# Performance work log

Measured on AMD Instinct MI355X. Metric: run time of the kernel, lower is better.

Reference implementation:

```python
import jax, jax.numpy as jnp
import numpy as np

N = 10000       # nodes
E = 160000      # edges
D_IN = 256      # in_channels (node feature dim)
H1, C = 8, 32   # conv1: 8 heads x 32 -> 256; conv2: 1 head x 32
MSG = 128       # msg_dim
TD = 128        # time encoder out_channels
ED = MSG + TD   # edge_dim = 256
HC1 = H1 * C    # 256


def _lin(key, shape, scale=0.05):
    return jax.random.normal(key, shape, dtype=jnp.float32) * scale


def setup_inputs() -> dict:
    key = jax.random.key(0)
    ks = jax.random.split(key, 32)
    inp = {}
    inp["x"] = jax.random.normal(ks[0], (N, D_IN), dtype=jnp.float32)
    inp["last_update"] = jax.random.uniform(ks[1], (N,), jnp.float32, 0.0, 1000.0)
    inp["edge_index"] = jax.random.randint(ks[2], (2, E), 0, N)
    inp["t"] = jax.random.uniform(ks[3], (E,), jnp.float32, 0.0, 1000.0)
    inp["msg"] = jax.random.normal(ks[4], (E, MSG), dtype=jnp.float32)
    # TimeEncoder: Linear(1, TD) then cos
    inp["time_w"] = _lin(ks[5], (TD, 1), 0.1)
    inp["time_b"] = jnp.zeros((TD,), jnp.float32)
    # conv1 (TransformerConv in=256, heads=8, per-head 32, edge_dim=256, concat=True)
    inp["Wq1"] = _lin(ks[6], (D_IN, HC1)); inp["bq1"] = jnp.zeros((HC1,), jnp.float32)
    inp["Wk1"] = _lin(ks[7], (D_IN, HC1)); inp["bk1"] = jnp.zeros((HC1,), jnp.float32)
    inp["Wv1"] = _lin(ks[8], (D_IN, HC1)); inp["bv1"] = jnp.zeros((HC1,), jnp.float32)
    inp["We1"] = _lin(ks[9], (ED, HC1))   # lin_edge has no bias in PyG
    inp["Ws1"] = _lin(ks[10], (D_IN, HC1)); inp["bs1"] = jnp.zeros((HC1,), jnp.float32)
    # conv2 (in=256, heads=1, per-head 32, concat=False)
    inp["Wq2"] = _lin(ks[11], (HC1, C)); inp["bq2"] = jnp.zeros((C,), jnp.float32)
    inp["Wk2"] = _lin(ks[12], (HC1, C)); inp["bk2"] = jnp.zeros((C,), jnp.float32)
    inp["Wv2"] = _lin(ks[13], (HC1, C)); inp["bv2"] = jnp.zeros((C,), jnp.float32)
    inp["We2"] = _lin(ks[14], (ED, C))
    inp["Ws2"] = _lin(ks[15], (HC1, C)); inp["bs2"] = jnp.zeros((C,), jnp.float32)
    return inp


def transformer_conv(x, src, dst, edge_attr, Wq, bq, Wk, bk, Wv, bv, We, Ws, bs, heads, ch, concat):
    n = x.shape[0]
    q = (x @ Wq + bq).reshape(n, heads, ch)
    k = (x @ Wk + bk).reshape(n, heads, ch)
    v = (x @ Wv + bv).reshape(n, heads, ch)
    e = (edge_attr @ We).reshape(-1, heads, ch)       # [E,H,C]
    ke = k[src] + e                                    # key_j + edge
    ve = v[src] + e                                    # value_j + edge
    alpha = jnp.einsum('ehc,ehc->eh', q[dst], ke) / jnp.sqrt(jnp.float32(ch))
    # segment softmax over incoming edges of each destination node
    amax = jax.ops.segment_max(alpha, dst, num_segments=n)   # -inf for empty segs
    ex = jnp.exp(alpha - amax[dst])
    den = jax.ops.segment_sum(ex, dst, num_segments=n)
    attn = ex / (den[dst] + 1e-16)                     # [E,H]
    out = jax.ops.segment_sum(attn[:, :, None] * ve, dst, num_segments=n)  # [N,H,C]
    out = out.reshape(n, heads * ch) if concat else out.mean(axis=1)
    return out + (x @ Ws + bs)                         # root skip connection


def reference(x, last_update, edge_index, t, msg, time_w, time_b,
              Wq1, bq1, Wk1, bk1, Wv1, bv1, We1, Ws1, bs1,
              Wq2, bq2, Wk2, bk2, Wv2, bv2, We2, Ws2, bs2):
    src, dst = edge_index[0], edge_index[1]
    rel_t = last_update[src] - t                       # [E]
    rel_t_enc = jnp.cos(rel_t[:, None] * time_w[:, 0][None, :] + time_b)  # [E,TD]
    edge_attr = jnp.concatenate([rel_t_enc, msg], axis=-1)                # [E,ED]
    h = jax.nn.relu(transformer_conv(x, src, dst, edge_attr,
                                     Wq1, bq1, Wk1, bk1, Wv1, bv1, We1, Ws1, bs1,
                                     H1, C, True))
    out = jax.nn.relu(transformer_conv(h, src, dst, edge_attr,
                                       Wq2, bq2, Wk2, bk2, Wv2, bv2, We2, Ws2, bs2,
                                       1, C, False))
    return out
```

## Files before the change

kernel.cpp:

```cpp
#include <hip/hip_runtime.h>
#include <math.h>

#define N_NODES 10000
#define N_EDGES 160000
#define RT1 157
#define RTE 2500
#define CONVX_T (RT1 * 64 * 32)
#define MAXSEG 16
#define SEGSTRIDE 576

static inline int ceildiv(int a, int b) { return (a + b - 1) / b; }

typedef float f32x4 __attribute__((ext_vector_type(4)));
typedef short bf16x8 __attribute__((ext_vector_type(8)));

__device__ __forceinline__ unsigned short f2bf(float f) {
  unsigned int u = __builtin_bit_cast(unsigned int, f);
  u += 0x7FFFu + ((u >> 16) & 1u);
  return (unsigned short)(u >> 16);
}
__device__ __forceinline__ float bf2f(unsigned short h) {
  unsigned int u = ((unsigned int)h) << 16;
  return __builtin_bit_cast(float, u);
}

__global__ void count_kernel(const int* __restrict__ dstp, int* __restrict__ deg, int E) {
  for (int i = blockIdx.x * blockDim.x + threadIdx.x; i < E; i += gridDim.x * blockDim.x)
    atomicAdd(&deg[dstp[i]], 1);
}

__global__ void scan_kernel(const int* __restrict__ deg, int* __restrict__ rowptr, int n) {
  __shared__ int part[1024];
  const int tid = threadIdx.x;
  const int CHK = 10;
  int base = tid * CHK;
  int loc[CHK];
  int s = 0;
#pragma unroll
  for (int j = 0; j < CHK; ++j) {
    int idx = base + j;
    int v = (idx < n) ? deg[idx] : 0;
    loc[j] = s; s += v;
  }
  part[tid] = s;
  __syncthreads();
  for (int off = 1; off < 1024; off <<= 1) {
    int y = (tid >= off) ? part[tid - off] : 0;
    __syncthreads();
    part[tid] += y;
    __syncthreads();
  }
  int pre = tid ? part[tid - 1] : 0;
#pragma unroll
  for (int j = 0; j < CHK; ++j) {
    int idx = base + j;
    if (idx < n) rowptr[idx] = pre + loc[j];
  }
  if (tid == 1023) rowptr[n] = part[1023];
}

__global__ void scatter_kernel(const float* __restrict__ lu, const float* __restrict__ tt,
                               const int* __restrict__ srcp, const int* __restrict__ dstp,
                               const int* __restrict__ rowptr, int* __restrict__ fill,
                               int* __restrict__ srcs, int* __restrict__ dsts,
                               int* __restrict__ eidA, float* __restrict__ rel_s, int E) {
  for (int e = blockIdx.x * blockDim.x + threadIdx.x; e < E; e += gridDim.x * blockDim.x) {
    int d = dstp[e], s = srcp[e];
    int pos = atomicAdd(&fill[d], 1);
    int slot = rowptr[d] + pos;
    srcs[slot] = s;
    dsts[slot] = d;
    eidA[slot] = e;
    rel_s[slot] = lu[s] - tt[e];
  }
}

__device__ __forceinline__ void wstore(const float* __restrict__ W, unsigned short* __restrict__ out,
                                       int Nin, int n_off, int NFtot, int k, int c) {
  int gc = n_off + c;
  int ks=k>>5, kg=(k>>3)&3, j=k&7, nf=gc>>4, ic=gc&15;
  out[(size_t)(ks*NFtot+nf)*512 + (ic+16*kg)*8 + j] = f2bf(W[(size_t)k*Nin + c]);
}

__global__ void conv_all_kernel(const float* __restrict__ x, unsigned short* __restrict__ xa,
                                const float* Wq1, const float* Wk1, const float* Wv1, const float* Ws1,
                                const float* We1, const float* Wq2, const float* Wk2, const float* Wv2,
                                const float* Ws2, const float* We2,
                                const float* bq1, const float* bk1, const float* bv1, const float* bs1,
                                const float* bq2, const float* bk2, const float* bv2, const float* bs2,
                                unsigned short* W1f, unsigned short* We1f, unsigned short* W2f,
                                unsigned short* We2f, float* bcat1, float* bcat2) {
  int t0 = blockIdx.x * blockDim.x + threadIdx.x;
  if (t0 < CONVX_T) {
    int i = t0 >> 5, k8 = t0 & 31;
    union { uint4 q; unsigned short s[8]; } u;
    if (i < N_NODES) {
      const float4* px = (const float4*)(x + (size_t)i * 256 + k8 * 8);
      float4 f0 = px[0], f1 = px[1];
      u.s[0]=f2bf(f0.x); u.s[1]=f2bf(f0.y); u.s[2]=f2bf(f0.z); u.s[3]=f2bf(f0.w);
      u.s[4]=f2bf(f1.x); u.s[5]=f2bf(f1.y); u.s[6]=f2bf(f1.z); u.s[7]=f2bf(f1.w);
    } else {
      u.q = make_uint4(0,0,0,0);
    }
    int rt=i>>6, rf=(i>>4)&3, ir=i&15, ks=k8>>2, kg=k8&3;
    *(uint4*)&xa[(size_t)rt*16384 + ks*2048 + rf*512 + (ir+16*kg)*8] = u.q;
    return;
  }
  int t = t0 - CONVX_T;
  if (t < 262144) {
    int w = t >> 16, r = t & 65535, k = r >> 8, c = r & 255;
    const float* W = (w == 0) ? Wq1 : (w == 1) ? Wk1 : (w == 2) ? Wv1 : Ws1;
    wstore(W, W1f, 256, w * 256, 64, k, c);
  } else if (t < 327680) {
    int r = t - 262144, k = r >> 8, c = r & 255;
    wstore(We1, We1f, 256, 0, 16, k, c);
  } else if (t < 360448) {
    int r = t - 327680, w = r >> 13, r2 = r & 8191, k = r2 >> 5, c = r2 & 31;
    const float* W = (w == 0) ? Wq2 : (w == 1) ? Wk2 : (w == 2) ? Wv2 : Ws2;
    wstore(W, W2f, 32, w * 32, 8, k, c);
  } else if (t < 368640) {
    int r = t - 360448, k = r >> 5, c = r & 31;
    wstore(We2, We2f, 32, 0, 4, k, c);
  } else if (t < 369792) {
    int r = t - 368640;
    if (r < 1024) {
      const float* b = (r < 256) ? bq1 : (r < 512) ? bk1 : (r < 768) ? bv1 : bs1;
      bcat1[r] = b[r & 255];
    } else {
      int r2 = r - 1024;
      const float* b = (r2 < 32) ? bq2 : (r2 < 64) ? bk2 : (r2 < 96) ? bv2 : bs2;
      bcat2[r2] = b[r2 & 31];
    }
  }
}

__global__ __launch_bounds__(512, 4)
void node1_gemm(const unsigned short* __restrict__ xa, const unsigned short* __restrict__ W1f,
                const float* __restrict__ bcat1, float* __restrict__ qf,
                unsigned short* __restrict__ kvb, float* __restrict__ sf) {
  __shared__ char ldsraw[32768];
  uint4* lds4 = (uint4*)ldsraw;
  const int tid = threadIdx.x;
  const int wid = tid >> 6, lane = tid & 63;
  const int fr0 = (lane >> 4) * 4;
  const int fc0 = lane & 15;
  const int rt0 = blockIdx.x % RT1;
  const int y = blockIdx.x / RT1;
  const int phase = rt0 & 7;

#pragma unroll
  for (int s = 0; s < 4; ++s)
    lds4[tid + s * 512] = *(const uint4*)(xa + (size_t)rt0 * 16384 + (size_t)(tid + s * 512) * 8);
  __syncthreads();

  f32x4 acc[4][2];
#pragma unroll
  for (int i = 0; i < 4; ++i)
#pragma unroll
    for (int j = 0; j < 2; ++j) acc[i][j] = (f32x4){0.f, 0.f, 0.f, 0.f};

  bf16x8 aN0, aN1, aN2, aN3, bN0, bN1;
  {
    const int ks = phase;
    aN0 = *(const bf16x8*)&lds4[ks * 256 + 0 * 64 + lane];
    aN1 = *(const bf16x8*)&lds4[ks * 256 + 1 * 64 + lane];
    aN2 = *(const bf16x8*)&lds4[ks * 256 + 2 * 64 + lane];
    aN3 = *(const bf16x8*)&lds4[ks * 256 + 3 * 64 + lane];
    bN0 = *(const bf16x8*)(W1f + ((size_t)(ks * 64 + y * 16 + wid * 2 + 0)) * 512 + (size_t)lane * 8);
    bN1 = *(const bf16x8*)(W1f + ((size_t)(ks * 64 + y * 16 + wid * 2 + 1)) * 512 + (size_t)lane * 8);
  }
#pragma unroll
  for (int ksi = 0; ksi < 8; ++ksi) {
    bf16x8 aC0 = aN0, aC1 = aN1, aC2 = aN2, aC3 = aN3;
    bf16x8 bC0 = bN0, bC1 = bN1;
    if (ksi < 7) {
      const int ks2 = (ksi + 1) ^ phase;
      aN0 = *(const bf16x8*)&lds4[ks2 * 256 + 0 * 64 + lane];
      aN1 = *(const bf16x8*)&lds4[ks2 * 256 + 1 * 64 + lane];
      aN2 = *(const bf16x8*)&lds4[ks2 * 256 + 2 * 64 + lane];
      aN3 = *(const bf16x8*)&lds4[ks2 * 256 + 3 * 64 + lane];
      bN0 = *(const bf16x8*)(W1f + ((size_t)(ks2 * 64 + y * 16 + wid * 2 + 0)) * 512 + (size_t)lane * 8);
      bN1 = *(const bf16x8*)(W1f + ((size_t)(ks2 * 64 + y * 16 + wid * 2 + 1)) * 512 + (size_t)lane * 8);
    }
    acc[0][0] = __builtin_amdgcn_mfma_f32_16x16x32_bf16(aC0, bC0, acc[0][0], 0, 0, 0);
    acc[1][0] = __builtin_amdgcn_mfma_f32_16x16x32_bf16(aC1, bC0, acc[1][0], 0, 0, 0);
    acc[2][0] = __builtin_amdgcn_mfma_f32_16x16x32_bf16(aC2, bC0, acc[2][0], 0, 0, 0);
    acc[3][0] = __builtin_amdgcn_mfma_f32_16x16x32_bf16(aC3, bC0, acc[3][0], 0, 0, 0);
    acc[0][1] = __builtin_amdgcn_mfma_f32_16x16x32_bf16(aC0, bC1, acc[0][1], 0, 0, 0);
    acc[1][1] = __builtin_amdgcn_mfma_f32_16x16x32_bf16(aC1, bC1, acc[1][1], 0, 0, 0);
    acc[2][1] = __builtin_amdgcn_mfma_f32_16x16x32_bf16(aC2, bC1, acc[2][1], 0, 0, 0);
    acc[3][1] = __builtin_amdgcn_mfma_f32_16x16x32_bf16(aC3, bC1, acc[3][1], 0, 0, 0);
  }

  bool bf16path;
  void* dstp_; int cstr_, dc0_, bcol0_;
  if (y == 0)      { bf16path = false; dstp_ = qf;  cstr_ = 256; dc0_ = 0;   bcol0_ = 0; }
  else if (y == 1) { bf16path = true;  dstp_ = kvb; cstr_ = 512; dc0_ = 0;   bcol0_ = 256; }
  else if (y == 2) { bf16path = true;  dstp_ = kvb; cstr_ = 512; dc0_ = 256; bcol0_ = 512; }
  else             { bf16path = false; dstp_ = sf;  cstr_ = 256; dc0_ = 0;   bcol0_ = 768; }
  if (!bf16path) {
    float* dst = (float*)dstp_;
    const int row0 = rt0 * 64 + fr0;
#pragma unroll
    for (int cf = 0; cf < 2; ++cf) {
      int c = wid * 32 + cf * 16 + fc0;
      float bv = bcat1[bcol0_ + c];
#pragma unroll
      for (int rf = 0; rf < 4; ++rf) {
#pragma unroll
        for (int j = 0; j < 4; ++j) {
          int r = row0 + rf * 16 + j;
          if (r < N_NODES) dst[(size_t)r * cstr_ + c] = acc[rf][cf][j] + bv;
        }
      }
    }
  } else {
    __syncthreads();
    unsigned short* cl = (unsigned short*)ldsraw;
    unsigned short* dst = (unsigned short*)dstp_;
    for (int pass = 0; pass < 4; ++pass) {
      if ((wid >> 1) == pass) {
#pragma unroll
        for (int cf = 0; cf < 2; ++cf) {
          int c = (wid & 1) * 32 + cf * 16 + fc0;
          float bv = bcat1[bcol0_ + pass * 64 + c];
#pragma unroll
          for (int rf = 0; rf < 4; ++rf)
#pragma unroll
            for (int j = 0; j < 4; ++j)
              cl[(fr0 + rf * 16 + j) * 72 + c] = f2bf(acc[rf][cf][j] + bv);
        }
      }
      __syncthreads();
      {
        int row = tid >> 3, cc = (tid & 7) * 8;
        int gr = rt0 * 64 + row;
        if (gr < N_NODES)
          *(uint4*)&dst[(size_t)gr * cstr_ + dc0_ + pass * 64 + cc] = *(const uint4*)&cl[row * 72 + cc];
      }
      __syncthreads();
    }
  }
}

__global__ __launch_bounds__(512, 4)
void edge_fused(const float* __restrict__ qf, const unsigned short* __restrict__ kvb,
                const unsigned short* __restrict__ We1f, const unsigned short* __restrict__ We2f,
                char* __restrict__ segrec, unsigned short* __restrict__ e2b,
                const float* __restrict__ rel_s, const float* __restrict__ tw,
                const float* __restrict__ tb, const float* __restrict__ msg,
                const int* __restrict__ eidA, const int* __restrict__ srcsA,
                const int* __restrict__ dstsA, const int* __restrict__ rowptr) {
  __shared__ char ldsraw[38912];
  uint4* lds4 = (uint4*)ldsraw;
  unsigned short* e1t = (unsigned short*)ldsraw;
  int* dseg     = (int*)(ldsraw + 33280);
  int* sseg     = (int*)(ldsraw + 33536);
  unsigned short* cl2 = (unsigned short*)(ldsraw + 33792);

  const int tid = threadIdx.x;
  const int wid = tid >> 6, lane = tid & 63;
  const int bx = blockIdx.x;
  const int fr0 = (lane >> 4) * 4;
  const int fc0 = lane & 15;
  const int rt0 = bx;
  const int phase = bx & 7;

  {
    const int rem = tid & 255;
    const int ksh = tid >> 8;
    const int arf = rem >> 6, ar2 = rem & 63, air = ar2 & 15, akg = ar2 >> 4;
    const int slot = rt0 * 64 + arf * 16 + air;
    float rl = rel_s[slot];
    int eorg = eidA[slot];
    if (tid < 64) {
      dseg[tid] = dstsA[rt0 * 64 + tid];
      sseg[tid] = srcsA[rt0 * 64 + tid];
    }
#pragma unroll
    for (int s = 0; s < 2; ++s) {
      int ks = ksh + s * 2;
      int k8 = ks * 4 + akg;
      const float4* twp = (const float4*)(tw + k8 * 8);
      const float4* tbp = (const float4*)(tb + k8 * 8);
      float4 w0 = twp[0], w1 = twp[1], b0 = tbp[0], b1 = tbp[1];
      union { uint4 q; unsigned short us[8]; } u;
      u.us[0]=f2bf(__cosf(rl*w0.x+b0.x)); u.us[1]=f2bf(__cosf(rl*w0.y+b0.y));
      u.us[2]=f2bf(__cosf(rl*w0.z+b0.z)); u.us[3]=f2bf(__cosf(rl*w0.w+b0.w));
      u.us[4]=f2bf(__cosf(rl*w1.x+b1.x)); u.us[5]=f2bf(__cosf(rl*w1.y+b1.y));
      u.us[6]=f2bf(__cosf(rl*w1.z+b1.z)); u.us[7]=f2bf(__cosf(rl*w1.w+b1.w));
      lds4[ks * 256 + rem] = u.q;
    }
#pragma unroll
    for (int s = 0; s < 2; ++s) {
      int ks = 4 + ksh + s * 2;
      int k8 = ks * 4 + akg;
      const float4* pm = (const float4*)(msg + (size_t)eorg * 128 + (size_t)(k8 - 16) * 8);
      float4 f0 = pm[0], f1 = pm[1];
      union { uint4 q; unsigned short us[8]; } u;
      u.us[0]=f2bf(f0.x); u.us[1]=f2bf(f0.y); u.us[2]=f2bf(f0.z); u.us[3]=f2bf(f0.w);
      u.us[4]=f2bf(f1.x); u.us[5]=f2bf(f1.y); u.us[6]=f2bf(f1.z); u.us[7]=f2bf(f1.w);
      lds4[ks * 256 + rem] = u.q;
    }
  }
  __syncthreads();

  f32x4 acc[4][2];
  f32x4 acc2[4];
#pragma unroll
  for (int i = 0; i < 4; ++i) {
    acc2[i] = (f32x4){0.f, 0.f, 0.f, 0.f};
#pragma unroll
    for (int j = 0; j < 2; ++j) acc[i][j] = (f32x4){0.f, 0.f, 0.f, 0.f};
  }

  bf16x8 aN0, aN1, aN2, aN3, bN0, bN1, b2N;
  {
    const int ks = phase;
    aN0 = *(const bf16x8*)&lds4[ks * 256 + 0 * 64 + lane];
    aN1 = *(const bf16x8*)&lds4[ks * 256 + 1 * 64 + lane];
    aN2 = *(const bf16x8*)&lds4[ks * 256 + 2 * 64 + lane];
    aN3 = *(const bf16x8*)&lds4[ks * 256 + 3 * 64 + lane];
    bN0 = *(const bf16x8*)(We1f + ((size_t)(ks * 16 + wid * 2 + 0)) * 512 + (size_t)lane * 8);
    bN1 = *(const bf16x8*)(We1f + ((size_t)(ks * 16 + wid * 2 + 1)) * 512 + (size_t)lane * 8);
    b2N = 0;
    if (wid < 2) b2N = *(const bf16x8*)(We2f + ((size_t)(ks * 4 + wid)) * 512 + (size_t)lane * 8);
  }
#pragma unroll
  for (int ksi = 0; ksi < 8; ++ksi) {
    bf16x8 aC0 = aN0, aC1 = aN1, aC2 = aN2, aC3 = aN3;
    bf16x8 bC0 = bN0, bC1 = bN1, b2C = b2N;
    if (ksi < 7) {
      const int ks2 = (ksi + 1) ^ phase;
      aN0 = *(const bf16x8*)&lds4[ks2 * 256 + 0 * 64 + lane];
      aN1 = *(const bf16x8*)&lds4[ks2 * 256 + 1 * 64 + lane];
      aN2 = *(const bf16x8*)&lds4[ks2 * 256 + 2 * 64 + lane];
      aN3 = *(const bf16x8*)&lds4[ks2 * 256 + 3 * 64 + lane];
      bN0 = *(const bf16x8*)(We1f + ((size_t)(ks2 * 16 + wid * 2 + 0)) * 512 + (size_t)lane * 8);
      bN1 = *(const bf16x8*)(We1f + ((size_t)(ks2 * 16 + wid * 2 + 1)) * 512 + (size_t)lane * 8);
      if (wid < 2) b2N = *(const bf16x8*)(We2f + ((size_t)(ks2 * 4 + wid)) * 512 + (size_t)lane * 8);
    }
    acc[0][0] = __builtin_amdgcn_mfma_f32_16x16x32_bf16(aC0, bC0, acc[0][0], 0, 0, 0);
    acc[1][0] = __builtin_amdgcn_mfma_f32_16x16x32_bf16(aC1, bC0, acc[1][0], 0, 0, 0);
    acc[2][0] = __builtin_amdgcn_mfma_f32_16x16x32_bf16(aC2, bC0, acc[2][0], 0, 0, 0);
    acc[3][0] = __builtin_amdgcn_mfma_f32_16x16x32_bf16(aC3, bC0, acc[3][0], 0, 0, 0);
    acc[0][1] = __builtin_amdgcn_mfma_f32_16x16x32_bf16(aC0, bC1, acc[0][1], 0, 0, 0);
    acc[1][1] = __builtin_amdgcn_mfma_f32_16x16x32_bf16(aC1, bC1, acc[1][1], 0, 0, 0);
    acc[2][1] = __builtin_amdgcn_mfma_f32_16x16x32_bf16(aC2, bC1, acc[2][1], 0, 0, 0);
    acc[3][1] = __builtin_amdgcn_mfma_f32_16x16x32_bf16(aC3, bC1, acc[3][1], 0, 0, 0);
    if (wid < 2) {
      acc2[0] = __builtin_amdgcn_mfma_f32_16x16x32_bf16(aC0, b2C, acc2[0], 0, 0, 0);
      acc2[1] = __builtin_amdgcn_mfma_f32_16x16x32_bf16(aC1, b2C, acc2[1], 0, 0, 0);
      acc2[2] = __builtin_amdgcn_mfma_f32_16x16x32_bf16(aC2, b2C, acc2[2], 0, 0, 0);
      acc2[3] = __builtin_amdgcn_mfma_f32_16x16x32_bf16(aC3, b2C, acc2[3], 0, 0, 0);
    }
  }

  __syncthreads();
#pragma unroll
  for (int cf = 0; cf < 2; ++cf)
#pragma unroll
    for (int rf = 0; rf < 4; ++rf)
#pragma unroll
      for (int j = 0; j < 4; ++j)
        e1t[(fr0 + rf * 16 + j) * 260 + wid * 32 + cf * 16 + fc0] = f2bf(acc[rf][cf][j]);
  if (wid < 2) {
#pragma unroll
    for (int rf = 0; rf < 4; ++rf)
#pragma unroll
      for (int j = 0; j < 4; ++j)
        cl2[(fr0 + rf * 16 + j) * 40 + wid * 16 + fc0] = f2bf(acc2[rf][j]);
  }
  __syncthreads();

  if (tid < 256) {
    int row = tid >> 2, cc = (tid & 3) * 8;
    *(uint4*)&e2b[(size_t)(rt0 * 64 + row) * 32 + cc] = *(const uint4*)&cl2[row * 40 + cc];
  }

  {
    const int base = wid * 8;
    const int rgj = bx * 8 + wid;
    int d8[8], s8[8];
#pragma unroll
    for (int t = 0; t < 8; ++t) { d8[t] = dseg[base + t]; s8[t] = sseg[base + t]; }

    ushort4 k8[8], e8[8];
#pragma unroll
    for (int t = 0; t < 8; ++t) {
      k8[t] = *(const ushort4*)&kvb[(size_t)s8[t] * 512 + lane * 4];
      e8[t] = *(const ushort4*)&e1t[(base + t) * 260 + lane * 4];
    }
    float4 q8[8];
    q8[0] = *(const float4*)&qf[(size_t)d8[0] * 256 + lane * 4];
#pragma unroll
    for (int t = 1; t < 8; ++t) {
      if (d8[t] == d8[t - 1]) q8[t] = q8[t - 1];
      else q8[t] = *(const float4*)&qf[(size_t)d8[t] * 256 + lane * 4];
    }
    float sc[8];
#pragma unroll
    for (int t = 0; t < 8; ++t) {
      float p = q8[t].x * (bf2f(k8[t].x) + bf2f(e8[t].x))
              + q8[t].y * (bf2f(k8[t].y) + bf2f(e8[t].y))
              + q8[t].z * (bf2f(k8[t].z) + bf2f(e8[t].z))
              + q8[t].w * (bf2f(k8[t].w) + bf2f(e8[t].w));
      p += __shfl_xor(p, 1); p += __shfl_xor(p, 2); p += __shfl_xor(p, 4);
      sc[t] = p * 0.17677669529663687f;
    }
    ushort4 v8[8];
#pragma unroll
    for (int t = 0; t < 8; ++t)
      v8[t] = *(const ushort4*)&kvb[(size_t)s8[t] * 512 + 256 + lane * 4];

    float m8[8], w8[8];
#pragma unroll
    for (int t = 0; t < 8; ++t) {
      float mm = sc[t];
#pragma unroll
      for (int u = 0; u < 8; ++u)
        if (d8[u] == d8[t]) mm = fmaxf(mm, sc[u]);
      m8[t] = mm;
      w8[t] = __expf(sc[t] - mm);
    }
#pragma unroll
    for (int t = 0; t < 8; ++t) {
      bool first = (t == 0) || (d8[t - 1] != d8[t]);
      if (first && (lane & 7) == 0) {
        float den = 0.f;
#pragma unroll
        for (int u = 0; u < 8; ++u)
          if (d8[u] == d8[t]) den += w8[u];
        int j = rgj - (rowptr[d8[t]] >> 3);
        if (j < MAXSEG) {
          float* rec = (float*)(segrec + ((size_t)d8[t] * MAXSEG + j) * SEGSTRIDE);
          rec[128 + (lane >> 3)] = m8[t];
          rec[136 + (lane >> 3)] = den;
        }
      }
    }
    f32x4 pacc = (f32x4){0.f, 0.f, 0.f, 0.f};
    int cur = d8[0];
#pragma unroll
    for (int t = 0; t < 8; ++t) {
      if (d8[t] != cur) {
        int j = rgj - (rowptr[cur] >> 3);
        if (j < MAXSEG) {
          unsigned short* pp = (unsigned short*)(segrec + ((size_t)cur * MAXSEG + j) * SEGSTRIDE);
          ushort4 o;
          o.x = f2bf(pacc[0]); o.y = f2bf(pacc[1]); o.z = f2bf(pacc[2]); o.w = f2bf(pacc[3]);
          *(ushort4*)&pp[lane * 4] = o;
        }
        pacc = (f32x4){0.f, 0.f, 0.f, 0.f};
        cur = d8[t];
      }
      pacc[0] += w8[t] * (bf2f(v8[t].x) + bf2f(e8[t].x));
      pacc[1] += w8[t] * (bf2f(v8[t].y) + bf2f(e8[t].y));
      pacc[2] += w8[t] * (bf2f(v8[t].z) + bf2f(e8[t].z));
      pacc[3] += w8[t] * (bf2f(v8[t].w) + bf2f(e8[t].w));
    }
    {
      int j = rgj - (rowptr[cur] >> 3);
      if (j < MAXSEG) {
        unsigned short* pp = (unsigned short*)(segrec + ((size_t)cur * MAXSEG + j) * SEGSTRIDE);
        ushort4 o;
        o.x = f2bf(pacc[0]); o.y = f2bf(pacc[1]); o.z = f2bf(pacc[2]); o.w = f2bf(pacc[3]);
        *(ushort4*)&pp[lane * 4] = o;
      }
    }
  }
}

__global__ __launch_bounds__(256)
void node2_fused(const char* __restrict__ segrec, const int* __restrict__ rowptr,
                 const float* __restrict__ sf, const unsigned short* __restrict__ W2f,
                 const float* __restrict__ bcat2, float* __restrict__ qkvs2) {
  __shared__ unsigned short haL[8 * 2048];
  const int tid = threadIdx.x;
  const int wid = tid >> 6, lane = tid & 63;
  const int rt0 = blockIdx.x;

  {
    const int nl = tid >> 2;
    const int n = rt0 * 64 + nl;
    const int cb = (tid & 3) * 64;
    const int rf = (nl >> 4) & 3, ir = nl & 15;
    if (n < N_NODES) {
      const int beg = rowptr[n], end = rowptr[n + 1];
      int span = 0;
      if (beg < end) {
        span = ((end - 1) >> 3) - (beg >> 3) + 1;
        if (span > MAXSEG) span = MAXSEG;
      }
#pragma unroll
      for (int cc = 0; cc < 4; ++cc) {
        const int c0 = cb + cc * 16;
        const int h = c0 >> 5;
        float o[16];
        if (span == 0) {
#pragma unroll
          for (int q = 0; q < 16; ++q) o[q] = 0.f;
        } else {
          float M = -INFINITY;
          for (int j = 0; j < span; ++j) {
            const float* rec = (const float*)(segrec + ((size_t)n * MAXSEG + j) * SEGSTRIDE);
            M = fmaxf(M, rec[128 + h]);
          }
          float den = 0.f;
#pragma unroll
          for (int q = 0; q < 16; ++q) o[q] = 0.f;
          for (int j = 0; j < span; ++j) {
            const float* rec = (const float*)(segrec + ((size_t)n * MAXSEG + j) * SEGSTRIDE);
            float scj = __expf(rec[128 + h] - M);
            den += scj * rec[136 + h];
            const unsigned short* pp = (const unsigned short*)rec;
#pragma unroll
            for (int q4 = 0; q4 < 4; ++q4) {
              ushort4 p4 = *(const ushort4*)&pp[c0 + q4 * 4];
              o[q4*4+0] += scj * bf2f(p4.x); o[q4*4+1] += scj * bf2f(p4.y);
              o[q4*4+2] += scj * bf2f(p4.z); o[q4*4+3] += scj * bf2f(p4.w);
            }
          }
          const float inv = 1.f / (den + 1e-16f);
#pragma unroll
          for (int q = 0; q < 16; ++q) o[q] *= inv;
        }
#pragma unroll
        for (int q4 = 0; q4 < 4; ++q4) {
          const int c = c0 + q4 * 4;
          float4 sk = *(const float4*)&sf[(size_t)n * 256 + c];
          ushort4 w4;
          w4.x = f2bf(fmaxf(o[q4*4+0] + sk.x, 0.f));
          w4.y = f2bf(fmaxf(o[q4*4+1] + sk.y, 0.f));
          w4.z = f2bf(fmaxf(o[q4*4+2] + sk.z, 0.f));
          w4.w = f2bf(fmaxf(o[q4*4+3] + sk.w, 0.f));
          int ks = c >> 5, kg = (c >> 3) & 3, j = c & 7;
          *(ushort4*)&haL[ks * 2048 + rf * 512 + (ir + 16 * kg) * 8 + j] = w4;
        }
      }
    } else {
#pragma unroll
      for (int cc = 0; cc < 4; ++cc) {
        const int c0 = cb + cc * 16;
#pragma unroll
        for (int q4 = 0; q4 < 4; ++q4) {
          const int c = c0 + q4 * 4;
          int ks = c >> 5, kg = (c >> 3) & 3, j = c & 7;
          ushort4 z; z.x = z.y = z.z = z.w = 0;
          *(ushort4*)&haL[ks * 2048 + rf * 512 + (ir + 16 * kg) * 8 + j] = z;
        }
      }
    }
  }
  __syncthreads();

  f32x4 acc[4][2];
#pragma unroll
  for (int i = 0; i < 4; ++i)
#pragma unroll
    for (int j = 0; j < 2; ++j) acc[i][j] = (f32x4){0.f, 0.f, 0.f, 0.f};

#pragma unroll
  for (int ks = 0; ks < 8; ++ks) {
    bf16x8 a[4], b[2];
#pragma unroll
    for (int rf = 0; rf < 4; ++rf)
      a[rf] = *(const bf16x8*)&haL[ks * 2048 + (rf * 64 + lane) * 8];
#pragma unroll
    for (int cf = 0; cf < 2; ++cf)
      b[cf] = *(const bf16x8*)(W2f + ((size_t)(ks * 8 + wid * 2 + cf)) * 512 + (size_t)lane * 8);
#pragma unroll
    for (int rf = 0; rf < 4; ++rf)
#pragma unroll
      for (int cf = 0; cf < 2; ++cf)
        acc[rf][cf] = __builtin_amdgcn_mfma_f32_16x16x32_bf16(a[rf], b[cf], acc[rf][cf], 0, 0, 0);
  }

  const int row0 = rt0 * 64 + ((lane >> 4) * 4);
  const int cb2 = wid * 32 + (lane & 15);
#pragma unroll
  for (int cf = 0; cf < 2; ++cf) {
    int c = cb2 + cf * 16;
    float bv = bcat2[c];
#pragma unroll
    for (int rf = 0; rf < 4; ++rf) {
#pragma unroll
      for (int j = 0; j < 4; ++j) {
        int r = row0 + rf * 16 + j;
        if (r < N_NODES) qkvs2[(size_t)r * 128 + c] = acc[rf][cf][j] + bv;
      }
    }
  }
}

__global__ __launch_bounds__(256)
void attn2_kernel(const float* __restrict__ qkvs2, const unsigned short* __restrict__ e2b,
                  const int* __restrict__ srcs, const int* __restrict__ rowptr,
                  float* __restrict__ outp) {
  const int n = blockIdx.x * 8 + (threadIdx.x >> 5);
  if (n >= N_NODES) return;
  const int c = threadIdx.x & 31;
  const int beg = rowptr[n], end = rowptr[n + 1];
  const float qv = qkvs2[(size_t)n * 128 + c];

  float m0=-INFINITY,d0=0,x0=0;
  float m1=-INFINITY,d1=0,x1=0;
  float m2=-INFINITY,d2=0,x2=0;
  float m3=-INFINITY,d3=0,x3=0;

  auto step = [&](int i, float& m, float& d, float& a) {
    const int s = srcs[i];
    const float ev = bf2f(e2b[(size_t)i * 32 + c]);
    float p = qv * (qkvs2[(size_t)s * 128 + 32 + c] + ev);
    const float v = qkvs2[(size_t)s * 128 + 64 + c] + ev;
#pragma unroll
    for (int off = 16; off; off >>= 1) p += __shfl_xor(p, off);
    p *= 0.17677669529663687f;
    const float mn = fmaxf(m, p);
    const float sc = __expf(m - mn), w = __expf(p - mn);
    d = d * sc + w; a = a * sc + w * v; m = mn;
  };

  int i = beg;
  for (; i + 3 < end; i += 4) {
    step(i, m0, d0, x0);
    step(i + 1, m1, d1, x1);
    step(i + 2, m2, d2, x2);
    step(i + 3, m3, d3, x3);
  }
  for (; i < end; ++i) step(i, m0, d0, x0);

  auto merge = [&](float& m, float& d, float& a, float mB, float dB, float b) {
    if (mB == -INFINITY) return;
    const float M = fmaxf(m, mB);
    const float sA = __expf(m - M), sB = __expf(mB - M);
    d = d * sA + dB * sB; a = a * sA + b * sB; m = M;
  };
  merge(m0, d0, x0, m1, d1, x1);
  merge(m2, d2, x2, m3, d3, x3);
  merge(m0, d0, x0, m2, d2, x2);

  float o = x0 / (d0 + 1e-16f) + qkvs2[(size_t)n * 128 + 96 + c];
  outp[(size_t)n * 32 + c] = fmaxf(o, 0.f);
}

extern "C" void kernel_launch(void* const* d_in, const int* in_sizes, int n_in,
                              void* d_out, int out_size, void* d_ws, size_t ws_size,
                              hipStream_t stream) {
  const float* x   = (const float*)d_in[0];
  const float* lu  = (const float*)d_in[1];
  const int*   ei  = (const int*)d_in[2];
  const float* tt  = (const float*)d_in[3];
  const float* msg = (const float*)d_in[4];
  const float* tw  = (const float*)d_in[5];
  const float* tb  = (const float*)d_in[6];
  const float* Wq1 = (const float*)d_in[7];  const float* bq1 = (const float*)d_in[8];
  const float* Wk1 = (const float*)d_in[9];  const float* bk1 = (const float*)d_in[10];
  const float* Wv1 = (const float*)d_in[11]; const float* bv1 = (const float*)d_in[12];
  const float* We1 = (const float*)d_in[13];
  const float* Ws1 = (const float*)d_in[14]; const float* bs1 = (const float*)d_in[15];
  const float* Wq2 = (const float*)d_in[16]; const float* bq2 = (const float*)d_in[17];
  const float* Wk2 = (const float*)d_in[18]; const float* bk2 = (const float*)d_in[19];
  const float* Wv2 = (const float*)d_in[20]; const float* bv2 = (const float*)d_in[21];
  const float* We2 = (const float*)d_in[22];
  const float* Ws2 = (const float*)d_in[23]; const float* bs2 = (const float*)d_in[24];

  const int* srcp = ei;
  const int* dstp = ei + N_EDGES;

  char* p = (char*)d_ws;
  auto alloc = [&](size_t bytes) -> char* {
    char* r = p;
    p += (bytes + 255) & ~(size_t)255;
    return r;
  };
  int*   deg     = (int*)alloc((size_t)N_NODES * 4);
  int*   fill    = (int*)alloc((size_t)N_NODES * 4);
  int*   rowptr  = (int*)alloc((size_t)(N_NODES + 1) * 4);
  int*   srcs    = (int*)alloc((size_t)N_EDGES * 4);
  int*   dsts    = (int*)alloc((size_t)N_EDGES * 4);
  int*   eidA    = (int*)alloc((size_t)N_EDGES * 4);
  float* rel_s   = (float*)alloc((size_t)N_EDGES * 4);
  unsigned short* xa   = (unsigned short*)alloc((size_t)RT1 * 32768);
  unsigned short* W1f  = (unsigned short*)alloc((size_t)8 * 64 * 1024);
  unsigned short* We1f = (unsigned short*)alloc((size_t)8 * 16 * 1024);
  unsigned short* W2f  = (unsigned short*)alloc((size_t)8 * 8 * 1024);
  unsigned short* We2f = (unsigned short*)alloc((size_t)8 * 4 * 1024);
  float* bcat1  = (float*)alloc(1024 * 4);
  float* bcat2  = (float*)alloc(128 * 4);
  float* qf     = (float*)alloc((size_t)N_NODES * 256 * 4);
  unsigned short* kvb = (unsigned short*)alloc((size_t)N_NODES * 512 * 2);
  float* sf     = (float*)alloc((size_t)N_NODES * 256 * 4);
  char*  segrec = (char*)alloc((size_t)N_NODES * MAXSEG * SEGSTRIDE);
  float* qkvs2  = (float*)alloc((size_t)N_NODES * 128 * 4);
  unsigned short* e2b = (unsigned short*)alloc((size_t)N_EDGES * 32 * 2);
  float* outp   = (float*)d_out;

  hipMemsetAsync(deg, 0, (size_t)N_NODES * 4, stream);
  hipMemsetAsync(fill, 0, (size_t)N_NODES * 4, stream);

  count_kernel<<<625, 256, 0, stream>>>(dstp, deg, N_EDGES);
  scan_kernel<<<1, 1024, 0, stream>>>(deg, rowptr, N_NODES);
  scatter_kernel<<<625, 256, 0, stream>>>(lu, tt, srcp, dstp, rowptr, fill,
                                          srcs, dsts, eidA, rel_s, N_EDGES);

  conv_all_kernel<<<ceildiv(CONVX_T + 369792, 256), 256, 0, stream>>>(
      x, xa, Wq1, Wk1, Wv1, Ws1, We1, Wq2, Wk2, Wv2, Ws2, We2,
      bq1, bk1, bv1, bs1, bq2, bk2, bv2, bs2,
      W1f, We1f, W2f, We2f, bcat1, bcat2);

  node1_gemm<<<RT1 * 4, 512, 0, stream>>>(xa, W1f, bcat1, qf, kvb, sf);

  edge_fused<<<RTE, 512, 0, stream>>>(
      qf, kvb, We1f, We2f, segrec, e2b,
      rel_s, tw, tb, msg, eidA, srcs, dsts, rowptr);

  node2_fused<<<RT1, 256, 0, stream>>>(segrec, rowptr, sf, W2f, bcat2, qkvs2);
  attn2_kernel<<<ceildiv(N_NODES, 8), 256, 0, stream>>>(qkvs2, e2b, srcs, rowptr, outp);
}
```

Before: 164.5 us.

## Convert x to bf16 inside node1 GEMM and merge degree count into weight conversion

The separate pass that converted node features to a bf16 tiled buffer is removed; node1_gemm now loads fp32 x rows directly, converts them, and writes the tiled layout into LDS. The degree-count kernel is merged into the weight-conversion kernel, saving one launch. The edge kernel also converts e values from bf16 once and reuses them for both the score and the value accumulation. The cost is that each of the four column-block groups of node1_gemm re-reads and re-converts the same fp32 x tile, doubling the bytes read per block.

```diff
diff --git a/kernel.cpp b/kernel.cpp
--- a/kernel.cpp
+++ b/kernel.cpp
@@ -5,7 +5,6 @@
 #define N_EDGES 160000
 #define RT1 157
 #define RTE 2500
-#define CONVX_T (RT1 * 64 * 32)
 #define MAXSEG 16
 #define SEGSTRIDE 576
 
@@ -22,11 +21,6 @@
 __device__ __forceinline__ float bf2f(unsigned short h) {
   unsigned int u = ((unsigned int)h) << 16;
   return __builtin_bit_cast(float, u);
-}
-
-__global__ void count_kernel(const int* __restrict__ dstp, int* __restrict__ deg, int E) {
-  for (int i = blockIdx.x * blockDim.x + threadIdx.x; i < E; i += gridDim.x * blockDim.x)
-    atomicAdd(&deg[dstp[i]], 1);
 }
 
 __global__ void scan_kernel(const int* __restrict__ deg, int* __restrict__ rowptr, int n) {
@@ -82,31 +76,20 @@
   out[(size_t)(ks*NFtot+nf)*512 + (ic+16*kg)*8 + j] = f2bf(W[(size_t)k*Nin + c]);
 }
 
-__global__ void conv_all_kernel(const float* __restrict__ x, unsigned short* __restrict__ xa,
-                                const float* Wq1, const float* Wk1, const float* Wv1, const float* Ws1,
-                                const float* We1, const float* Wq2, const float* Wk2, const float* Wv2,
-                                const float* Ws2, const float* We2,
-                                const float* bq1, const float* bk1, const float* bv1, const float* bs1,
-                                const float* bq2, const float* bk2, const float* bv2, const float* bs2,
-                                unsigned short* W1f, unsigned short* We1f, unsigned short* W2f,
-                                unsigned short* We2f, float* bcat1, float* bcat2) {
+__global__ void conv_w_count(const int* __restrict__ dstp, int* __restrict__ deg,
+                             const float* Wq1, const float* Wk1, const float* Wv1, const float* Ws1,
+                             const float* We1, const float* Wq2, const float* Wk2, const float* Wv2,
+                             const float* Ws2, const float* We2,
+                             const float* bq1, const float* bk1, const float* bv1, const float* bs1,
+                             const float* bq2, const float* bk2, const float* bv2, const float* bs2,
+                             unsigned short* W1f, unsigned short* We1f, unsigned short* W2f,
+                             unsigned short* We2f, float* bcat1, float* bcat2) {
   int t0 = blockIdx.x * blockDim.x + threadIdx.x;
-  if (t0 < CONVX_T) {
-    int i = t0 >> 5, k8 = t0 & 31;
-    union { uint4 q; unsigned short s[8]; } u;
-    if (i < N_NODES) {
-      const float4* px = (const float4*)(x + (size_t)i * 256 + k8 * 8);
-      float4 f0 = px[0], f1 = px[1];
-      u.s[0]=f2bf(f0.x); u.s[1]=f2bf(f0.y); u.s[2]=f2bf(f0.z); u.s[3]=f2bf(f0.w);
-      u.s[4]=f2bf(f1.x); u.s[5]=f2bf(f1.y); u.s[6]=f2bf(f1.z); u.s[7]=f2bf(f1.w);
-    } else {
-      u.q = make_uint4(0,0,0,0);
-    }
-    int rt=i>>6, rf=(i>>4)&3, ir=i&15, ks=k8>>2, kg=k8&3;
-    *(uint4*)&xa[(size_t)rt*16384 + ks*2048 + rf*512 + (ir+16*kg)*8] = u.q;
+  if (t0 < N_EDGES) {
+    atomicAdd(&deg[dstp[t0]], 1);
     return;
   }
-  int t = t0 - CONVX_T;
+  int t = t0 - N_EDGES;
   if (t < 262144) {
     int w = t >> 16, r = t & 65535, k = r >> 8, c = r & 255;
     const float* W = (w == 0) ? Wq1 : (w == 1) ? Wk1 : (w == 2) ? Wv1 : Ws1;
@@ -135,7 +118,7 @@
 }
 
 __global__ __launch_bounds__(512, 4)
-void node1_gemm(const unsigned short* __restrict__ xa, const unsigned short* __restrict__ W1f,
+void node1_gemm(const float* __restrict__ x, const unsigned short* __restrict__ W1f,
                 const float* __restrict__ bcat1, float* __restrict__ qf,
                 unsigned short* __restrict__ kvb, float* __restrict__ sf) {
   __shared__ char ldsraw[32768];
@@ -148,9 +131,29 @@
   const int y = blockIdx.x / RT1;
   const int phase = rt0 & 7;
 
-#pragma unroll
-  for (int s = 0; s < 4; ++s)
-    lds4[tid + s * 512] = *(const uint4*)(xa + (size_t)rt0 * 16384 + (size_t)(tid + s * 512) * 8);
+  {
+    const int row = tid >> 3;
+    const int t8 = tid & 7;
+    const int gr = rt0 * 64 + row;
+    const int rf = (row >> 4) & 3, ir = row & 15;
+    float4 xv[8];
+    if (gr < N_NODES) {
+      const float4* px = (const float4*)(x + (size_t)gr * 256 + t8 * 32);
+#pragma unroll
+      for (int q = 0; q < 8; ++q) xv[q] = px[q];
+    } else {
+#pragma unroll
+      for (int q = 0; q < 8; ++q) xv[q] = make_float4(0.f, 0.f, 0.f, 0.f);
+    }
+#pragma unroll
+    for (int kg = 0; kg < 4; ++kg) {
+      union { uint4 u; unsigned short us[8]; } w;
+      float4 a = xv[kg * 2], b = xv[kg * 2 + 1];
+      w.us[0]=f2bf(a.x); w.us[1]=f2bf(a.y); w.us[2]=f2bf(a.z); w.us[3]=f2bf(a.w);
+      w.us[4]=f2bf(b.x); w.us[5]=f2bf(b.y); w.us[6]=f2bf(b.z); w.us[7]=f2bf(b.w);
+      lds4[t8 * 256 + rf * 64 + ir + 16 * kg] = w.u;
+    }
+  }
   __syncthreads();
 
   f32x4 acc[4][2];
@@ -391,6 +394,12 @@
       k8[t] = *(const ushort4*)&kvb[(size_t)s8[t] * 512 + lane * 4];
       e8[t] = *(const ushort4*)&e1t[(base + t) * 260 + lane * 4];
     }
+    float ef[8][4];
+#pragma unroll
+    for (int t = 0; t < 8; ++t) {
+      ef[t][0] = bf2f(e8[t].x); ef[t][1] = bf2f(e8[t].y);
+      ef[t][2] = bf2f(e8[t].z); ef[t][3] = bf2f(e8[t].w);
+    }
     float4 q8[8];
     q8[0] = *(const float4*)&qf[(size_t)d8[0] * 256 + lane * 4];
 #pragma unroll
@@ -401,10 +410,10 @@
     float sc[8];
 #pragma unroll
     for (int t = 0; t < 8; ++t) {
-      float p = q8[t].x * (bf2f(k8[t].x) + bf2f(e8[t].x))
-              + q8[t].y * (bf2f(k8[t].y) + bf2f(e8[t].y))
-              + q8[t].z * (bf2f(k8[t].z) + bf2f(e8[t].z))
-              + q8[t].w * (bf2f(k8[t].w) + bf2f(e8[t].w));
+      float p = q8[t].x * (bf2f(k8[t].x) + ef[t][0])
+              + q8[t].y * (bf2f(k8[t].y) + ef[t][1])
+              + q8[t].z * (bf2f(k8[t].z) + ef[t][2])
+              + q8[t].w * (bf2f(k8[t].w) + ef[t][3]);
       p += __shfl_xor(p, 1); p += __shfl_xor(p, 2); p += __shfl_xor(p, 4);
       sc[t] = p * 0.17677669529663687f;
     }
@@ -454,10 +463,10 @@
         pacc = (f32x4){0.f, 0.f, 0.f, 0.f};
         cur = d8[t];
       }
-      pacc[0] += w8[t] * (bf2f(v8[t].x) + bf2f(e8[t].x));
-      pacc[1] += w8[t] * (bf2f(v8[t].y) + bf2f(e8[t].y));
-      pacc[2] += w8[t] * (bf2f(v8[t].z) + bf2f(e8[t].z));
-      pacc[3] += w8[t] * (bf2f(v8[t].w) + bf2f(e8[t].w));
+      pacc[0] += w8[t] * (bf2f(v8[t].x) + ef[t][0]);
+      pacc[1] += w8[t] * (bf2f(v8[t].y) + ef[t][1]);
+      pacc[2] += w8[t] * (bf2f(v8[t].z) + ef[t][2]);
+      pacc[3] += w8[t] * (bf2f(v8[t].w) + ef[t][3]);
     }
     {
       int j = rgj - (rowptr[cur] >> 3);
@@ -681,7 +690,6 @@
   int*   dsts    = (int*)alloc((size_t)N_EDGES * 4);
   int*   eidA    = (int*)alloc((size_t)N_EDGES * 4);
   float* rel_s   = (float*)alloc((size_t)N_EDGES * 4);
-  unsigned short* xa   = (unsigned short*)alloc((size_t)RT1 * 32768);
   unsigned short* W1f  = (unsigned short*)alloc((size_t)8 * 64 * 1024);
   unsigned short* We1f = (unsigned short*)alloc((size_t)8 * 16 * 1024);
   unsigned short* W2f  = (unsigned short*)alloc((size_t)8 * 8 * 1024);
@@ -699,17 +707,17 @@
   hipMemsetAsync(deg, 0, (size_t)N_NODES * 4, stream);
   hipMemsetAsync(fill, 0, (size_t)N_NODES * 4, stream);
 
-  count_kernel<<<625, 256, 0, stream>>>(dstp, deg, N_EDGES);
+  conv_w_count<<<ceildiv(N_EDGES + 369792, 256), 256, 0, stream>>>(
+      dstp, deg,
+      Wq1, Wk1, Wv1, Ws1, We1, Wq2, Wk2, Wv2, Ws2, We2,
+      bq1, bk1, bv1, bs1, bq2, bk2, bv2, bs2,
+      W1f, We1f, W2f, We2f, bcat1, bcat2);
+
   scan_kernel<<<1, 1024, 0, stream>>>(deg, rowptr, N_NODES);
   scatter_kernel<<<625, 256, 0, stream>>>(lu, tt, srcp, dstp, rowptr, fill,
                                           srcs, dsts, eidA, rel_s, N_EDGES);
 
-  conv_all_kernel<<<ceildiv(CONVX_T + 369792, 256), 256, 0, stream>>>(
-      x, xa, Wq1, Wk1, Wv1, Ws1, We1, Wq2, Wk2, Wv2, Ws2, We2,
-      bq1, bk1, bv1, bs1, bq2, bk2, bv2, bs2,
-      W1f, We1f, W2f, We2f, bcat1, bcat2);
-
-  node1_gemm<<<RT1 * 4, 512, 0, stream>>>(xa, W1f, bcat1, qf, kvb, sf);
+  node1_gemm<<<RT1 * 4, 512, 0, stream>>>(x, W1f, bcat1, qf, kvb, sf);
 
   edge_fused<<<RTE, 512, 0, stream>>>(
       qf, kvb, We1f, We2f, segrec, e2b,
```

After: 166.3 us. Within noise of the previous version (+1.1%).
